# Performance work log

Hardware: AMD Instinct MI355X
Metric: run time of the kernel (lower is better)

Reference implementation:

```python
import jax, jax.numpy as jnp
import numpy as np

N = 50000      # nodes
E = 800000     # edges
F_IN = 256     # feat_dim
H = 256        # hidden dim (both layers)
L = 128        # latent dim
BN_EPS = 1e-5


def setup_inputs() -> dict:
    key = jax.random.key(0)
    ks = jax.random.split(key, 16)
    x = jax.random.normal(ks[0], (N, F_IN), dtype=jnp.float32)
    edge_index = jax.random.randint(ks[1], (2, E), 0, N, dtype=jnp.int32)
    s = 0.05
    return {
        "x": x,
        "edge_index": edge_index,
        "W0": s * jax.random.normal(ks[2], (F_IN, H), jnp.float32),
        "b0": jnp.zeros((H,), jnp.float32),
        "gamma0": jnp.ones((H,), jnp.float32),
        "beta0": jnp.zeros((H,), jnp.float32),
        "W1": s * jax.random.normal(ks[3], (H, H), jnp.float32),
        "b1": jnp.zeros((H,), jnp.float32),
        "gamma1": jnp.ones((H,), jnp.float32),
        "beta1": jnp.zeros((H,), jnp.float32),
        "W_mu": s * jax.random.normal(ks[4], (H, L), jnp.float32),
        "b_mu": jnp.zeros((L,), jnp.float32),
        "W_lv": s * jax.random.normal(ks[5], (H, L), jnp.float32),
        "b_lv": jnp.zeros((L,), jnp.float32),
    }


def _gcn_conv(h, src, dst, coef, W, b):
    # h' = W h, then symmetric-normalized scatter-add aggregation (PyG GCNConv)
    h = h @ W                                   # [N, H]
    msg = h[src] * coef                         # gather + scale, [E+N, H]
    out = jax.ops.segment_sum(msg, dst, num_segments=N)
    return out + b


def _bn(h, gamma, beta):
    # BatchNorm1d over node dimension (training-mode batch statistics)
    m = h.mean(axis=0)
    v = h.var(axis=0)
    return (h - m) * jax.lax.rsqrt(v + BN_EPS) * gamma + beta


def reference(x, edge_index, W0, b0, gamma0, beta0, W1, b1, gamma1, beta1,
              W_mu, b_mu, W_lv, b_lv):
    loops = jnp.arange(N, dtype=edge_index.dtype)
    src = jnp.concatenate([edge_index[0], loops])   # with self-loops
    dst = jnp.concatenate([edge_index[1], loops])
    deg = jax.ops.segment_sum(jnp.ones((E + N,), x.dtype), dst, num_segments=N)
    dinv = jnp.where(deg > 0, jax.lax.rsqrt(jnp.maximum(deg, 1.0)), 0.0)
    coef = (dinv[src] * dinv[dst])[:, None]          # [E+N, 1]

    h = jax.nn.relu(_bn(_gcn_conv(x, src, dst, coef, W0, b0), gamma0, beta0))
    h = jax.nn.relu(_bn(_gcn_conv(h, src, dst, coef, W1, b1), gamma1, beta1))
    # dropout is identity at inference
    mu = h @ W_mu + b_mu
    logvar = h @ W_lv + b_lv
    return mu, logvar
```

## Files before the change

### kernel.cpp

```cpp
#include <hip/hip_runtime.h>
#include <hip/hip_bf16.h>

#define NN 50000
#define NP 50001
#define NE 800000
#define FD 256
#define LD 128
#define BN_EPS 1e-5f
#define NEPAD (NE + 7 * NN + 16)

typedef __bf16 bf16_t;
typedef bf16_t bf16x8 __attribute__((ext_vector_type(8)));
typedef float f32x4 __attribute__((ext_vector_type(4)));
typedef float f32x2 __attribute__((ext_vector_type(2)));
typedef int i32x2 __attribute__((ext_vector_type(2)));
typedef int i32x4 __attribute__((ext_vector_type(4)));
typedef unsigned int u32x4 __attribute__((ext_vector_type(4)));
typedef unsigned short u16x8 __attribute__((ext_vector_type(8)));


__global__ __launch_bounds__(256) void k_count(const int* __restrict__ dst,
                                               int* __restrict__ cnt) {
  int i = blockIdx.x * blockDim.x + threadIdx.x;
  if (i < NE) atomicAdd(&cnt[dst[i]], 1);
}

__global__ __launch_bounds__(256) void k_scanA(const int* __restrict__ cnt,
                                               int* __restrict__ row_ptr,
                                               int* __restrict__ partials) {
  __shared__ int ws[4];
  int b = blockIdx.x, t = threadIdx.x;
  int base = b * 1024 + t * 4;
  int vals[4];
#pragma unroll
  for (int j = 0; j < 4; ++j)
    vals[j] = (base + j < NN) ? ((cnt[base + j] + 7) & ~7) : 0;
  int tsum = vals[0] + vals[1] + vals[2] + vals[3];
  int lane = t & 63, wid = t >> 6;
  int x = tsum;
#pragma unroll
  for (int off = 1; off < 64; off <<= 1) {
    int y = __shfl_up(x, off, 64);
    if (lane >= off) x += y;
  }
  if (lane == 63) ws[wid] = x;
  __syncthreads();
  int woff = 0;
  for (int w = 0; w < wid; ++w) woff += ws[w];
  int run = woff + x - tsum;
#pragma unroll
  for (int j = 0; j < 4; ++j) {
    if (base + j < NN) row_ptr[base + j] = run;
    run += vals[j];
  }
  if (t == 255) partials[b] = woff + x;
}

__global__ void k_scanB(int* __restrict__ partials, int* __restrict__ row_ptr,
                        int nblk) {
  int lane = threadIdx.x;
  int v = (lane < nblk) ? partials[lane] : 0;
  int x = v;
#pragma unroll
  for (int off = 1; off < 64; off <<= 1) {
    int y = __shfl_up(x, off, 64);
    if (lane >= off) x += y;
  }
  if (lane < nblk) partials[lane] = x - v;
  if (lane == nblk - 1) row_ptr[NN] = x;
}

__global__ __launch_bounds__(256) void k_scanC(int* __restrict__ row_ptr,
                                               const int* __restrict__ partials,
                                               const int* __restrict__ cnt,
                                               float* __restrict__ dinv,
                                               unsigned short* __restrict__ col,
                                               int* __restrict__ hist) {
  __shared__ int lh[64];
  int b = blockIdx.x, t = threadIdx.x;
  if (t < 64) lh[t] = 0;
  __syncthreads();
  int off = partials[b];
  int base = b * 1024 + t * 4;
#pragma unroll
  for (int j = 0; j < 4; ++j)
    if (base + j < NN) {
      int deg = cnt[base + j];
      int rp = row_ptr[base + j] + off;
      row_ptr[base + j] = rp;
      dinv[base + j] = rsqrtf(1.0f + (float)deg);
      int pd = (deg + 7) & ~7;
      for (int p = deg; p < pd; ++p) col[rp + p] = (unsigned short)NN;
      int it = pd >> 3;
      if (it > 63) it = 63;
      atomicAdd(&lh[it], 1);
    }
  __syncthreads();
  if (t < 64 && lh[t]) atomicAdd(&hist[t], lh[t]);
}

__global__ __launch_bounds__(256) void k_fill(const int* __restrict__ src,
                                              const int* __restrict__ dst,
                                              const int* __restrict__ row_ptr,
                                              int* __restrict__ cursor,
                                              unsigned short* __restrict__ col) {
  int i = blockIdx.x * blockDim.x + threadIdx.x;
  if (i < NE) {
    int d = dst[i];
    int p = atomicAdd(&cursor[d], 1);
    col[row_ptr[d] + p] = (unsigned short)src[i];
  }
}

__global__ __launch_bounds__(256) void k_order(
    const int* __restrict__ cnt, const int* __restrict__ row_ptr,
    const float* __restrict__ dinv, const int* __restrict__ hist,
    int* __restrict__ rank, int* __restrict__ order, i32x2* __restrict__ desc,
    float* __restrict__ dinvp) {
  __shared__ int lcnt[64];
  __shared__ int gbase[64];
  __shared__ int sc[64];
  int t = threadIdx.x;
  if (t < 64) {
    lcnt[t] = 0;
    int v = hist[t];
    int x = v;
#pragma unroll
    for (int off = 1; off < 64; off <<= 1) {
      int y = __shfl_up(x, off, 64);
      if (t >= off) x += y;
    }
    sc[t] = x - v;
  }
  __syncthreads();
  int i = blockIdx.x * 256 + t;
  int it = 0, rloc = 0, pd = 0;
  bool valid = (i < NN);
  if (valid) {
    pd = (cnt[i] + 7) & ~7;
    it = pd >> 3;
    if (it > 63) it = 63;
    rloc = atomicAdd(&lcnt[it], 1);
  }
  __syncthreads();
  if (t < 64 && lcnt[t]) gbase[t] = sc[t] + atomicAdd(&rank[t], lcnt[t]);
  __syncthreads();
  if (valid) {
    int p = gbase[it] + rloc;
    order[p] = i;
    int rp = row_ptr[i];
    desc[p] = (i32x2){rp, rp + pd};
    dinvp[p] = dinv[i];
  }
}

__global__ __launch_bounds__(256) void k_convw(
    const float* __restrict__ W0, const float* __restrict__ W1,
    const float* __restrict__ Wmu, const float* __restrict__ bmu,
    const float* __restrict__ Wlv, const float* __restrict__ blv,
    bf16_t* __restrict__ W0s, bf16_t* __restrict__ W1s,
    bf16_t* __restrict__ Whs, float* __restrict__ biash,
    bf16_t* __restrict__ g16, bf16_t* __restrict__ agg16) {
  int k = blockIdx.x, n = threadIdx.x;
  int chunk = (n >> 4) * 8 + (k >> 5);
  int slot = ((k >> 3) & 3) * 16 + (n & 15);
  int idx = chunk * 512 + slot * 8 + (k & 7);
  W0s[idx] = (bf16_t)W0[k * 256 + n];
  W1s[idx] = (bf16_t)W1[k * 256 + n];
  float wh = (n < 128) ? Wmu[k * 128 + n] : Wlv[k * 128 + (n - 128)];
  Whs[idx] = (bf16_t)wh;
  if (k == 0) biash[n] = (n < 128) ? bmu[n] : blv[n - 128];
  if (k == 1) {
    int ss = n >> 6, j = n & 63;
    g16[((size_t)ss * NP + NN) * 64 + j] = (bf16_t)0.f;
    agg16[((size_t)ss * NP + NN) * 64 + j] = (bf16_t)0.f;
  }
}

__global__ __launch_bounds__(256) void k_mgemm(
    const void* __restrict__ Ap, int a_f32, const bf16_t* __restrict__ Wswz,
    bf16_t* __restrict__ Cb, float* __restrict__ Cf, int M,
    const float* __restrict__ stats, const float* __restrict__ gamma,
    const float* __restrict__ beta, const float* __restrict__ row_scale,
    const float* __restrict__ col_bias, int split) {
  __shared__ float bnsc_l[256], bnsh_l[256];
  const int tid = threadIdx.x;
  const int half = blockIdx.y;
  if (stats) {
    float mean = stats[tid] * (1.0f / NN);
    float var = stats[256 + tid] * (1.0f / NN) - mean * mean;
    float rs = rsqrtf(var + BN_EPS);
    float sc = gamma[tid] * rs;
    bnsc_l[tid] = sc;
    bnsh_l[tid] = beta[tid] - mean * sc;
    __syncthreads();
  }

  const int wave = tid >> 6, lane = tid & 63;
  const int m = lane & 15, q = lane >> 4;
  const int row0 = blockIdx.x * 64 + wave * 16;
  const int rg = row0 + m;
  const int rc = rg < M ? rg : M - 1;

  bf16x8 af[8];
  if (a_f32) {
    const float* p = (const float*)Ap + (size_t)rc * 256 + q * 8;
    float4 f0[8], f1[8];
#pragma unroll
    for (int kb = 0; kb < 8; ++kb) {
      f0[kb] = *(const float4*)(p + kb * 32);
      f1[kb] = *(const float4*)(p + kb * 32 + 4);
    }
#pragma unroll
    for (int kb = 0; kb < 8; ++kb) {
      bf16x8 fr;
      fr[0] = (bf16_t)f0[kb].x; fr[1] = (bf16_t)f0[kb].y;
      fr[2] = (bf16_t)f0[kb].z; fr[3] = (bf16_t)f0[kb].w;
      fr[4] = (bf16_t)f1[kb].x; fr[5] = (bf16_t)f1[kb].y;
      fr[6] = (bf16_t)f1[kb].z; fr[7] = (bf16_t)f1[kb].w;
      af[kb] = fr;
    }
  } else {
    const bf16_t* pA = (const bf16_t*)Ap;
    bf16x8 raw[8];
#pragma unroll
    for (int kb = 0; kb < 8; ++kb)
      raw[kb] = *(const bf16x8*)&pA[((size_t)(kb >> 1) * NP + rc) * 64 +
                                    (kb & 1) * 32 + q * 8];
#pragma unroll
    for (int kb = 0; kb < 8; ++kb) {
      float s[8], h[8];
      if (stats) {
        float4 s0 = *(const float4*)&bnsc_l[kb * 32 + q * 8];
        float4 s1 = *(const float4*)&bnsc_l[kb * 32 + q * 8 + 4];
        float4 h0 = *(const float4*)&bnsh_l[kb * 32 + q * 8];
        float4 h1 = *(const float4*)&bnsh_l[kb * 32 + q * 8 + 4];
        s[0] = s0.x; s[1] = s0.y; s[2] = s0.z; s[3] = s0.w;
        s[4] = s1.x; s[5] = s1.y; s[6] = s1.z; s[7] = s1.w;
        h[0] = h0.x; h[1] = h0.y; h[2] = h0.z; h[3] = h0.w;
        h[4] = h1.x; h[5] = h1.y; h[6] = h1.z; h[7] = h1.w;
      }
      bf16x8 r = raw[kb];
      bf16x8 fr;
#pragma unroll
      for (int j = 0; j < 8; ++j) {
        float v = (float)r[j];
        if (stats) v = fmaxf(fmaf(v, s[j], h[j]), 0.f);
        fr[j] = (bf16_t)v;
      }
      af[kb] = fr;
    }
  }

  const bf16_t* Wb = Wswz + (size_t)half * 64 * 512 + lane * 8;
  f32x4 acc[8] = {};
#pragma unroll
  for (int nt = 0; nt < 8; ++nt) {
#pragma unroll
    for (int kb = 0; kb < 8; ++kb) {
      bf16x8 b = *(const bf16x8*)&Wb[(nt * 8 + kb) * 512];
      acc[nt] =
          __builtin_amdgcn_mfma_f32_16x16x32_bf16(af[kb], b, acc[nt], 0, 0, 0);
    }
  }

#pragma unroll
  for (int r = 0; r < 4; ++r) {
    int row = row0 + q * 4 + r;
    if (row >= M) continue;
    float rs = row_scale ? row_scale[row] : 1.0f;
#pragma unroll
    for (int nt = 0; nt < 8; ++nt) {
      int col = half * 128 + nt * 16 + m;
      float v = acc[nt][r] * rs;
      if (col_bias) v += col_bias[col];
      if (Cb) {
        Cb[((size_t)(col >> 6) * NP + row) * 64 + (col & 63)] = (bf16_t)v;
      } else if (!split) {
        Cf[(size_t)row * 256 + col] = v;
      } else {
        if (col < 128)
          Cf[(size_t)row * 128 + col] = v;
        else
          Cf[(size_t)(M + row) * 128 + (col - 128)] = v;
      }
    }
  }
}

#define ACCUM8(A, d)                                             \
  A[0] += (f32x2){__uint_as_float(d[0] << 16),                   \
                  __uint_as_float(d[0] & 0xffff0000u)};          \
  A[1] += (f32x2){__uint_as_float(d[1] << 16),                   \
                  __uint_as_float(d[1] & 0xffff0000u)};          \
  A[2] += (f32x2){__uint_as_float(d[2] << 16),                   \
                  __uint_as_float(d[2] & 0xffff0000u)};          \
  A[3] += (f32x2){__uint_as_float(d[3] << 16),                   \
                  __uint_as_float(d[3] & 0xffff0000u)};

__global__ __launch_bounds__(256) void k_spmm(
    const bf16_t* __restrict__ g, const int* __restrict__ order,
    const i32x2* __restrict__ desc, const unsigned short* __restrict__ col,
    const float* __restrict__ dinvp, bf16_t* __restrict__ out,
    float* __restrict__ stats) {
  __shared__ float sbuf[32][64];
  const int s = blockIdx.x & 3;
  const int grp = blockIdx.x >> 2;
  const int team = threadIdx.x >> 3, tl = threadIdx.x & 7;
  const int slotA = grp * 64 + team * 2;
  const u32x4* gu = (const u32x4*)(g + (size_t)s * NP * 64);
  float s1[8] = {}, s2[8] = {};
  if (slotA < NN) {
    f32x2 accA[4] = {}, accB[4] = {};
    i32x2 o2 = *(const i32x2*)&order[slotA];
    i32x4 d4 = *(const i32x4*)&desc[slotA];
    f32x2 dv2 = *(const f32x2*)&dinvp[slotA];
    int dstA = o2[0], dstB = o2[1];
    int bA = d4[0], eA = d4[1], bB = d4[2], eB = d4[3];
    {
      u32x4 dA = gu[(size_t)dstA * 8 + tl];
      u32x4 dB = gu[(size_t)dstB * 8 + tl];
      ACCUM8(accA, dA)
      ACCUM8(accB, dB)
    }
    u16x8 cA = {}, cB = {};
    if (bA < eA) cA = __builtin_nontemporal_load((const u16x8*)&col[bA]);
    if (bB < eB) cB = __builtin_nontemporal_load((const u16x8*)&col[bB]);
    while (bA < eA && bB < eB) {
      u32x4 wa0 = gu[(size_t)cA[0] * 8 + tl];
      u32x4 wa1 = gu[(size_t)cA[1] * 8 + tl];
      u32x4 wa2 = gu[(size_t)cA[2] * 8 + tl];
      u32x4 wa3 = gu[(size_t)cA[3] * 8 + tl];
      u32x4 wa4 = gu[(size_t)cA[4] * 8 + tl];
      u32x4 wa5 = gu[(size_t)cA[5] * 8 + tl];
      u32x4 wa6 = gu[(size_t)cA[6] * 8 + tl];
      u32x4 wa7 = gu[(size_t)cA[7] * 8 + tl];
      u32x4 wb0 = gu[(size_t)cB[0] * 8 + tl];
      u32x4 wb1 = gu[(size_t)cB[1] * 8 + tl];
      u32x4 wb2 = gu[(size_t)cB[2] * 8 + tl];
      u32x4 wb3 = gu[(size_t)cB[3] * 8 + tl];
      u32x4 wb4 = gu[(size_t)cB[4] * 8 + tl];
      u32x4 wb5 = gu[(size_t)cB[5] * 8 + tl];
      u32x4 wb6 = gu[(size_t)cB[6] * 8 + tl];
      u32x4 wb7 = gu[(size_t)cB[7] * 8 + tl];
      int bnA = bA + 8, bnB = bB + 8;
      u16x8 cnA = {}, cnB = {};
      if (bnA < eA) cnA = __builtin_nontemporal_load((const u16x8*)&col[bnA]);
      if (bnB < eB) cnB = __builtin_nontemporal_load((const u16x8*)&col[bnB]);
      ACCUM8(accA, wa0) ACCUM8(accA, wa1) ACCUM8(accA, wa2) ACCUM8(accA, wa3)
      ACCUM8(accA, wa4) ACCUM8(accA, wa5) ACCUM8(accA, wa6) ACCUM8(accA, wa7)
      ACCUM8(accB, wb0) ACCUM8(accB, wb1) ACCUM8(accB, wb2) ACCUM8(accB, wb3)
      ACCUM8(accB, wb4) ACCUM8(accB, wb5) ACCUM8(accB, wb6) ACCUM8(accB, wb7)
      cA = cnA;
      cB = cnB;
      bA = bnA;
      bB = bnB;
    }
    while (bA < eA) {
      u32x4 w0 = gu[(size_t)cA[0] * 8 + tl];
      u32x4 w1 = gu[(size_t)cA[1] * 8 + tl];
      u32x4 w2 = gu[(size_t)cA[2] * 8 + tl];
      u32x4 w3 = gu[(size_t)cA[3] * 8 + tl];
      u32x4 w4 = gu[(size_t)cA[4] * 8 + tl];
      u32x4 w5 = gu[(size_t)cA[5] * 8 + tl];
      u32x4 w6 = gu[(size_t)cA[6] * 8 + tl];
      u32x4 w7 = gu[(size_t)cA[7] * 8 + tl];
      int bn = bA + 8;
      u16x8 cn = {};
      if (bn < eA) cn = __builtin_nontemporal_load((const u16x8*)&col[bn]);
      ACCUM8(accA, w0) ACCUM8(accA, w1) ACCUM8(accA, w2) ACCUM8(accA, w3)
      ACCUM8(accA, w4) ACCUM8(accA, w5) ACCUM8(accA, w6) ACCUM8(accA, w7)
      cA = cn;
      bA = bn;
    }
    while (bB < eB) {
      u32x4 w0 = gu[(size_t)cB[0] * 8 + tl];
      u32x4 w1 = gu[(size_t)cB[1] * 8 + tl];
      u32x4 w2 = gu[(size_t)cB[2] * 8 + tl];
      u32x4 w3 = gu[(size_t)cB[3] * 8 + tl];
      u32x4 w4 = gu[(size_t)cB[4] * 8 + tl];
      u32x4 w5 = gu[(size_t)cB[5] * 8 + tl];
      u32x4 w6 = gu[(size_t)cB[6] * 8 + tl];
      u32x4 w7 = gu[(size_t)cB[7] * 8 + tl];
      int bn = bB + 8;
      u16x8 cn = {};
      if (bn < eB) cn = __builtin_nontemporal_load((const u16x8*)&col[bn]);
      ACCUM8(accB, w0) ACCUM8(accB, w1) ACCUM8(accB, w2) ACCUM8(accB, w3)
      ACCUM8(accB, w4) ACCUM8(accB, w5) ACCUM8(accB, w6) ACCUM8(accB, w7)
      cB = cn;
      bB = bn;
    }
    float dvA = dv2[0], dvB = dv2[1];
    bf16x8 ovA, ovB;
#pragma unroll
    for (int j = 0; j < 8; ++j) {
      ovA[j] = (bf16_t)(accA[j >> 1][j & 1] * dvA);
      ovB[j] = (bf16_t)(accB[j >> 1][j & 1] * dvB);
    }
    __builtin_nontemporal_store(
        ovA, (bf16x8*)&out[((size_t)s * NP + dstA) * 64 + (size_t)tl * 8]);
    __builtin_nontemporal_store(
        ovB, (bf16x8*)&out[((size_t)s * NP + dstB) * 64 + (size_t)tl * 8]);
#pragma unroll
    for (int j = 0; j < 8; ++j) {
      float va = (float)ovA[j], vb = (float)ovB[j];
      s1[j] += va + vb;
      s2[j] = fmaf(va, va, s2[j]);
      s2[j] = fmaf(vb, vb, s2[j]);
    }
  }
#pragma unroll
  for (int j = 0; j < 8; ++j) sbuf[team][tl * 8 + j] = s1[j];
  __syncthreads();
  if (threadIdx.x < 64) {
    float tot = 0.f;
#pragma unroll
    for (int w = 0; w < 32; ++w) tot += sbuf[w][threadIdx.x];
    atomicAdd(&stats[s * 64 + threadIdx.x], tot);
  }
  __syncthreads();
#pragma unroll
  for (int j = 0; j < 8; ++j) sbuf[team][tl * 8 + j] = s2[j];
  __syncthreads();
  if (threadIdx.x < 64) {
    float tot = 0.f;
#pragma unroll
    for (int w = 0; w < 32; ++w) tot += sbuf[w][threadIdx.x];
    atomicAdd(&stats[256 + s * 64 + threadIdx.x], tot);
  }
}

extern "C" void kernel_launch(void* const* d_in, const int* in_sizes, int n_in,
                              void* d_out, int out_size, void* d_ws, size_t ws_size,
                              hipStream_t stream) {
  const float* x = (const float*)d_in[0];
  const int* ei = (const int*)d_in[1];
  const int* esrc = ei;
  const int* edst = ei + NE;
  const float* W0 = (const float*)d_in[2];
  const float* gamma0 = (const float*)d_in[4];
  const float* beta0 = (const float*)d_in[5];
  const float* W1 = (const float*)d_in[6];
  const float* gamma1 = (const float*)d_in[8];
  const float* beta1 = (const float*)d_in[9];
  const float* W_mu = (const float*)d_in[10];
  const float* b_mu = (const float*)d_in[11];
  const float* W_lv = (const float*)d_in[12];
  const float* b_lv = (const float*)d_in[13];
  float* out = (float*)d_out;

  bf16_t* g16 = (bf16_t*)d_ws;
  bf16_t* agg16 = g16 + (size_t)4 * NP * 64;
  int* cnt = (int*)(agg16 + (size_t)4 * NP * 64);
  int* cursor = cnt + NN;
  float* statsAll = (float*)(cursor + NN);
  int* hist = (int*)(statsAll + 1024);
  int* rank = hist + 64;
  float* dinv = (float*)(rank + 64);
  float* biash = dinv + NN;
  bf16_t* W0s = (bf16_t*)(biash + 256);
  bf16_t* W1s = W0s + 256 * 256;
  bf16_t* Whs = W1s + 256 * 256;
  int* row_ptr = (int*)(Whs + 256 * 256);
  int* order = row_ptr + NN + 4;
  float* dinvp = (float*)(order + NN);
  i32x2* desc = (i32x2*)(dinvp + NN);
  unsigned short* col = (unsigned short*)(desc + NN);
  int* partials = (int*)(col + NEPAD);

  const int SCAN_BLKS = (NN + 1023) / 1024;

  hipMemsetAsync(cnt, 0, (2 * NN + 1024 + 128) * sizeof(int), stream);
  k_count<<<(NE + 255) / 256, 256, 0, stream>>>(edst, cnt);
  k_scanA<<<SCAN_BLKS, 256, 0, stream>>>(cnt, row_ptr, partials);
  k_scanB<<<1, 64, 0, stream>>>(partials, row_ptr, SCAN_BLKS);
  k_scanC<<<SCAN_BLKS, 256, 0, stream>>>(row_ptr, partials, cnt, dinv, col,
                                         hist);
  k_fill<<<(NE + 255) / 256, 256, 0, stream>>>(esrc, edst, row_ptr, cursor, col);
  k_order<<<(NN + 255) / 256, 256, 0, stream>>>(cnt, row_ptr, dinv, hist, rank,
                                                order, desc, dinvp);
  k_convw<<<256, 256, 0, stream>>>(W0, W1, W_mu, b_mu, W_lv, b_lv, W0s, W1s,
                                   Whs, biash, g16, agg16);

  dim3 gg((NN + 63) / 64, 2);
  const int SPMM_BLKS = 4 * ((NN + 63) / 64);

  k_mgemm<<<gg, 256, 0, stream>>>(x, 1, W0s, g16, nullptr, NN, nullptr, nullptr,
                                  nullptr, dinv, nullptr, 0);
  k_spmm<<<SPMM_BLKS, 256, 0, stream>>>(g16, order, desc, col, dinvp, agg16,
                                        statsAll);

  k_mgemm<<<gg, 256, 0, stream>>>(agg16, 0, W1s, g16, nullptr, NN, statsAll,
                                  gamma0, beta0, dinv, nullptr, 0);
  k_spmm<<<SPMM_BLKS, 256, 0, stream>>>(g16, order, desc, col, dinvp, agg16,
                                        statsAll + 512);

  k_mgemm<<<gg, 256, 0, stream>>>(agg16, 0, Whs, nullptr, out, NN,
                                  statsAll + 512, gamma1, beta1, nullptr, biash,
                                  1);
}
```

Measured before the change: 402.3 us.

## Fuse CSR build preprocessing kernels into one cooperative grid-synced kernel

```diff
diff --git a/kernel.cpp b/kernel.cpp
--- a/kernel.cpp
+++ b/kernel.cpp
@@ -1,5 +1,8 @@
 #include <hip/hip_runtime.h>
 #include <hip/hip_bf16.h>
+#include <hip/hip_cooperative_groups.h>
+
+namespace cg = cooperative_groups;
 
 #define NN 50000
 #define NP 50001
@@ -18,162 +21,149 @@
 typedef unsigned int u32x4 __attribute__((ext_vector_type(4)));
 typedef unsigned short u16x8 __attribute__((ext_vector_type(8)));
 
-
-__global__ __launch_bounds__(256) void k_count(const int* __restrict__ dst,
-                                               int* __restrict__ cnt) {
-  int i = blockIdx.x * blockDim.x + threadIdx.x;
-  if (i < NE) atomicAdd(&cnt[dst[i]], 1);
-}
-
-__global__ __launch_bounds__(256) void k_scanA(const int* __restrict__ cnt,
-                                               int* __restrict__ row_ptr,
-                                               int* __restrict__ partials) {
-  __shared__ int ws[4];
-  int b = blockIdx.x, t = threadIdx.x;
-  int base = b * 1024 + t * 4;
-  int vals[4];
-#pragma unroll
-  for (int j = 0; j < 4; ++j)
-    vals[j] = (base + j < NN) ? ((cnt[base + j] + 7) & ~7) : 0;
-  int tsum = vals[0] + vals[1] + vals[2] + vals[3];
-  int lane = t & 63, wid = t >> 6;
-  int x = tsum;
-#pragma unroll
-  for (int off = 1; off < 64; off <<= 1) {
-    int y = __shfl_up(x, off, 64);
-    if (lane >= off) x += y;
-  }
-  if (lane == 63) ws[wid] = x;
+__global__ __launch_bounds__(256) void k_build(
+    const int* __restrict__ src, const int* __restrict__ dst,
+    int* __restrict__ cnt, int* __restrict__ cursor, int* __restrict__ row_ptr,
+    int* __restrict__ partials, float* __restrict__ dinv,
+    unsigned short* __restrict__ col, int* __restrict__ hist,
+    int* __restrict__ rank, int* __restrict__ order, i32x2* __restrict__ desc,
+    float* __restrict__ dinvp, const float* __restrict__ W0,
+    const float* __restrict__ W1, const float* __restrict__ Wmu,
+    const float* __restrict__ bmu, const float* __restrict__ Wlv,
+    const float* __restrict__ blv, bf16_t* __restrict__ W0s,
+    bf16_t* __restrict__ W1s, bf16_t* __restrict__ Whs,
+    float* __restrict__ biash, bf16_t* __restrict__ g16,
+    bf16_t* __restrict__ agg16) {
+  cg::grid_group grid = cg::this_grid();
+  __shared__ int s0[64], s1[64], s2[64];
+  const int t = threadIdx.x, b = blockIdx.x;
+  const int gtid = b * 256 + t;
+  const int GT = 256 * 256;
+
+  for (int i = gtid; i < 2 * NN + 1152; i += GT) cnt[i] = 0;
+  {
+    int k = b, n = t;
+    int chunk = (n >> 4) * 8 + (k >> 5);
+    int slot = ((k >> 3) & 3) * 16 + (n & 15);
+    int idx = chunk * 512 + slot * 8 + (k & 7);
+    W0s[idx] = (bf16_t)W0[k * 256 + n];
+    W1s[idx] = (bf16_t)W1[k * 256 + n];
+    float wh = (n < 128) ? Wmu[k * 128 + n] : Wlv[k * 128 + (n - 128)];
+    Whs[idx] = (bf16_t)wh;
+    if (k == 0) biash[n] = (n < 128) ? bmu[n] : blv[n - 128];
+    if (k == 1) {
+      int ss = n >> 6, j = n & 63;
+      g16[((size_t)ss * NP + NN) * 64 + j] = (bf16_t)0.f;
+      agg16[((size_t)ss * NP + NN) * 64 + j] = (bf16_t)0.f;
+    }
+  }
+  grid.sync();
+
+  for (int i = gtid; i < NE; i += GT) atomicAdd(&cnt[dst[i]], 1);
+  grid.sync();
+
+  if (b < 49) {
+    int base = b * 1024 + t * 4;
+    int vals[4];
+#pragma unroll
+    for (int j = 0; j < 4; ++j)
+      vals[j] = (base + j < NN) ? ((cnt[base + j] + 7) & ~7) : 0;
+    int tsum = vals[0] + vals[1] + vals[2] + vals[3];
+    int lane = t & 63, wid = t >> 6;
+    int x = tsum;
+#pragma unroll
+    for (int off = 1; off < 64; off <<= 1) {
+      int y = __shfl_up(x, off, 64);
+      if (lane >= off) x += y;
+    }
+    if (lane == 63) s0[wid] = x;
+    __syncthreads();
+    int woff = 0;
+    for (int w = 0; w < wid; ++w) woff += s0[w];
+    int run = woff + x - tsum;
+#pragma unroll
+    for (int j = 0; j < 4; ++j) {
+      if (base + j < NN) row_ptr[base + j] = run;
+      run += vals[j];
+    }
+    if (t == 255) partials[b] = woff + x;
+  }
+  grid.sync();
+
+  if (b == 0 && t < 64) {
+    int v = (t < 49) ? partials[t] : 0;
+    int x = v;
+#pragma unroll
+    for (int off = 1; off < 64; off <<= 1) {
+      int y = __shfl_up(x, off, 64);
+      if (t >= off) x += y;
+    }
+    if (t < 49) partials[t] = x - v;
+    if (t == 48) row_ptr[NN] = x;
+  }
+  grid.sync();
+
+  if (t < 64) s0[t] = 0;
   __syncthreads();
-  int woff = 0;
-  for (int w = 0; w < wid; ++w) woff += ws[w];
-  int run = woff + x - tsum;
-#pragma unroll
-  for (int j = 0; j < 4; ++j) {
-    if (base + j < NN) row_ptr[base + j] = run;
-    run += vals[j];
-  }
-  if (t == 255) partials[b] = woff + x;
-}
-
-__global__ void k_scanB(int* __restrict__ partials, int* __restrict__ row_ptr,
-                        int nblk) {
-  int lane = threadIdx.x;
-  int v = (lane < nblk) ? partials[lane] : 0;
-  int x = v;
-#pragma unroll
-  for (int off = 1; off < 64; off <<= 1) {
-    int y = __shfl_up(x, off, 64);
-    if (lane >= off) x += y;
-  }
-  if (lane < nblk) partials[lane] = x - v;
-  if (lane == nblk - 1) row_ptr[NN] = x;
-}
-
-__global__ __launch_bounds__(256) void k_scanC(int* __restrict__ row_ptr,
-                                               const int* __restrict__ partials,
-                                               const int* __restrict__ cnt,
-                                               float* __restrict__ dinv,
-                                               unsigned short* __restrict__ col,
-                                               int* __restrict__ hist) {
-  __shared__ int lh[64];
-  int b = blockIdx.x, t = threadIdx.x;
-  if (t < 64) lh[t] = 0;
-  __syncthreads();
-  int off = partials[b];
-  int base = b * 1024 + t * 4;
-#pragma unroll
-  for (int j = 0; j < 4; ++j)
-    if (base + j < NN) {
-      int deg = cnt[base + j];
-      int rp = row_ptr[base + j] + off;
-      row_ptr[base + j] = rp;
-      dinv[base + j] = rsqrtf(1.0f + (float)deg);
-      int pd = (deg + 7) & ~7;
-      for (int p = deg; p < pd; ++p) col[rp + p] = (unsigned short)NN;
+  if (b < 49) {
+    int off = partials[b];
+    int base = b * 1024 + t * 4;
+#pragma unroll
+    for (int j = 0; j < 4; ++j)
+      if (base + j < NN) {
+        int deg = cnt[base + j];
+        int rp = row_ptr[base + j] + off;
+        row_ptr[base + j] = rp;
+        dinv[base + j] = rsqrtf(1.0f + (float)deg);
+        int pd = (deg + 7) & ~7;
+        for (int p = deg; p < pd; ++p) col[rp + p] = (unsigned short)NN;
+        int it = pd >> 3;
+        if (it > 63) it = 63;
+        atomicAdd(&s0[63 - it], 1);
+      }
+    __syncthreads();
+    if (t < 64 && s0[t]) atomicAdd(&hist[t], s0[t]);
+  }
+  grid.sync();
+
+  {
+    if (t < 64) {
+      s0[t] = 0;
+      int v = hist[t];
+      int x = v;
+#pragma unroll
+      for (int off = 1; off < 64; off <<= 1) {
+        int y = __shfl_up(x, off, 64);
+        if (t >= off) x += y;
+      }
+      s2[t] = x - v;
+    }
+    __syncthreads();
+    int i = gtid;
+    int bin = 0, rloc = 0, pd = 0;
+    bool valid = (i < NN);
+    if (valid) {
+      pd = (cnt[i] + 7) & ~7;
       int it = pd >> 3;
       if (it > 63) it = 63;
-      atomicAdd(&lh[it], 1);
-    }
-  __syncthreads();
-  if (t < 64 && lh[t]) atomicAdd(&hist[t], lh[t]);
-}
-
-__global__ __launch_bounds__(256) void k_fill(const int* __restrict__ src,
-                                              const int* __restrict__ dst,
-                                              const int* __restrict__ row_ptr,
-                                              int* __restrict__ cursor,
-                                              unsigned short* __restrict__ col) {
-  int i = blockIdx.x * blockDim.x + threadIdx.x;
-  if (i < NE) {
+      bin = 63 - it;
+      rloc = atomicAdd(&s0[bin], 1);
+    }
+    __syncthreads();
+    if (t < 64 && s0[t]) s1[t] = s2[t] + atomicAdd(&rank[t], s0[t]);
+    __syncthreads();
+    if (valid) {
+      int p = s1[bin] + rloc;
+      order[p] = i;
+      int rp = row_ptr[i];
+      desc[p] = (i32x2){rp, rp + pd};
+      dinvp[p] = dinv[i];
+    }
+  }
+  for (int i = gtid; i < NE; i += GT) {
     int d = dst[i];
     int p = atomicAdd(&cursor[d], 1);
     col[row_ptr[d] + p] = (unsigned short)src[i];
-  }
-}
-
-__global__ __launch_bounds__(256) void k_order(
-    const int* __restrict__ cnt, const int* __restrict__ row_ptr,
-    const float* __restrict__ dinv, const int* __restrict__ hist,
-    int* __restrict__ rank, int* __restrict__ order, i32x2* __restrict__ desc,
-    float* __restrict__ dinvp) {
-  __shared__ int lcnt[64];
-  __shared__ int gbase[64];
-  __shared__ int sc[64];
-  int t = threadIdx.x;
-  if (t < 64) {
-    lcnt[t] = 0;
-    int v = hist[t];
-    int x = v;
-#pragma unroll
-    for (int off = 1; off < 64; off <<= 1) {
-      int y = __shfl_up(x, off, 64);
-      if (t >= off) x += y;
-    }
-    sc[t] = x - v;
-  }
-  __syncthreads();
-  int i = blockIdx.x * 256 + t;
-  int it = 0, rloc = 0, pd = 0;
-  bool valid = (i < NN);
-  if (valid) {
-    pd = (cnt[i] + 7) & ~7;
-    it = pd >> 3;
-    if (it > 63) it = 63;
-    rloc = atomicAdd(&lcnt[it], 1);
-  }
-  __syncthreads();
-  if (t < 64 && lcnt[t]) gbase[t] = sc[t] + atomicAdd(&rank[t], lcnt[t]);
-  __syncthreads();
-  if (valid) {
-    int p = gbase[it] + rloc;
-    order[p] = i;
-    int rp = row_ptr[i];
-    desc[p] = (i32x2){rp, rp + pd};
-    dinvp[p] = dinv[i];
-  }
-}
-
-__global__ __launch_bounds__(256) void k_convw(
-    const float* __restrict__ W0, const float* __restrict__ W1,
-    const float* __restrict__ Wmu, const float* __restrict__ bmu,
-    const float* __restrict__ Wlv, const float* __restrict__ blv,
-    bf16_t* __restrict__ W0s, bf16_t* __restrict__ W1s,
-    bf16_t* __restrict__ Whs, float* __restrict__ biash,
-    bf16_t* __restrict__ g16, bf16_t* __restrict__ agg16) {
-  int k = blockIdx.x, n = threadIdx.x;
-  int chunk = (n >> 4) * 8 + (k >> 5);
-  int slot = ((k >> 3) & 3) * 16 + (n & 15);
-  int idx = chunk * 512 + slot * 8 + (k & 7);
-  W0s[idx] = (bf16_t)W0[k * 256 + n];
-  W1s[idx] = (bf16_t)W1[k * 256 + n];
-  float wh = (n < 128) ? Wmu[k * 128 + n] : Wlv[k * 128 + (n - 128)];
-  Whs[idx] = (bf16_t)wh;
-  if (k == 0) biash[n] = (n < 128) ? bmu[n] : blv[n - 128];
-  if (k == 1) {
-    int ss = n >> 6, j = n & 63;
-    g16[((size_t)ss * NP + NN) * 64 + j] = (bf16_t)0.f;
-    agg16[((size_t)ss * NP + NN) * 64 + j] = (bf16_t)0.f;
   }
 }
 
@@ -468,19 +458,14 @@
   unsigned short* col = (unsigned short*)(desc + NN);
   int* partials = (int*)(col + NEPAD);
 
-  const int SCAN_BLKS = (NN + 1023) / 1024;
-
-  hipMemsetAsync(cnt, 0, (2 * NN + 1024 + 128) * sizeof(int), stream);
-  k_count<<<(NE + 255) / 256, 256, 0, stream>>>(edst, cnt);
-  k_scanA<<<SCAN_BLKS, 256, 0, stream>>>(cnt, row_ptr, partials);
-  k_scanB<<<1, 64, 0, stream>>>(partials, row_ptr, SCAN_BLKS);
-  k_scanC<<<SCAN_BLKS, 256, 0, stream>>>(row_ptr, partials, cnt, dinv, col,
-                                         hist);
-  k_fill<<<(NE + 255) / 256, 256, 0, stream>>>(esrc, edst, row_ptr, cursor, col);
-  k_order<<<(NN + 255) / 256, 256, 0, stream>>>(cnt, row_ptr, dinv, hist, rank,
-                                                order, desc, dinvp);
-  k_convw<<<256, 256, 0, stream>>>(W0, W1, W_mu, b_mu, W_lv, b_lv, W0s, W1s,
-                                   Whs, biash, g16, agg16);
+  {
+    void* args[] = {&esrc, &edst, &cnt,   &cursor, &row_ptr, &partials, &dinv,
+                    &col,  &hist, &rank,  &order,  &desc,    &dinvp,    &W0,
+                    &W1,   &W_mu, &b_mu,  &W_lv,   &b_lv,    &W0s,      &W1s,
+                    &Whs,  &biash, &g16,  &agg16};
+    hipLaunchCooperativeKernel((void*)k_build, dim3(256), dim3(256), args, 0,
+                               stream);
+  }
 
   dim3 gg((NN + 63) / 64, 2);
   const int SPMM_BLKS = 4 * ((NN + 63) / 64);
```

New measurement: 553.6 us. 37.6% more time.

## Fuse CSR build kernels, single-block scan, stage GEMM weights in LDS

Applied to the files above, without the earlier changes.

```diff
diff --git a/kernel.cpp b/kernel.cpp
--- a/kernel.cpp
+++ b/kernel.cpp
@@ -8,6 +8,8 @@
 #define LD 128
 #define BN_EPS 1e-5f
 #define NEPAD (NE + 7 * NN + 16)
+#define CNT_BLKS 3125
+#define ORD_BLKS 196
 
 typedef __bf16 bf16_t;
 typedef bf16_t bf16x8 __attribute__((ext_vector_type(8)));
@@ -18,187 +20,178 @@
 typedef unsigned int u32x4 __attribute__((ext_vector_type(4)));
 typedef unsigned short u16x8 __attribute__((ext_vector_type(8)));
 
-
-__global__ __launch_bounds__(256) void k_count(const int* __restrict__ dst,
-                                               int* __restrict__ cnt) {
-  int i = blockIdx.x * blockDim.x + threadIdx.x;
-  if (i < NE) atomicAdd(&cnt[dst[i]], 1);
-}
-
-__global__ __launch_bounds__(256) void k_scanA(const int* __restrict__ cnt,
-                                               int* __restrict__ row_ptr,
-                                               int* __restrict__ partials) {
-  __shared__ int ws[4];
-  int b = blockIdx.x, t = threadIdx.x;
-  int base = b * 1024 + t * 4;
-  int vals[4];
-#pragma unroll
-  for (int j = 0; j < 4; ++j)
-    vals[j] = (base + j < NN) ? ((cnt[base + j] + 7) & ~7) : 0;
-  int tsum = vals[0] + vals[1] + vals[2] + vals[3];
-  int lane = t & 63, wid = t >> 6;
-  int x = tsum;
-#pragma unroll
-  for (int off = 1; off < 64; off <<= 1) {
-    int y = __shfl_up(x, off, 64);
-    if (lane >= off) x += y;
-  }
-  if (lane == 63) ws[wid] = x;
-  __syncthreads();
-  int woff = 0;
-  for (int w = 0; w < wid; ++w) woff += ws[w];
-  int run = woff + x - tsum;
-#pragma unroll
-  for (int j = 0; j < 4; ++j) {
-    if (base + j < NN) row_ptr[base + j] = run;
-    run += vals[j];
-  }
-  if (t == 255) partials[b] = woff + x;
-}
-
-__global__ void k_scanB(int* __restrict__ partials, int* __restrict__ row_ptr,
-                        int nblk) {
-  int lane = threadIdx.x;
-  int v = (lane < nblk) ? partials[lane] : 0;
-  int x = v;
-#pragma unroll
-  for (int off = 1; off < 64; off <<= 1) {
-    int y = __shfl_up(x, off, 64);
-    if (lane >= off) x += y;
-  }
-  if (lane < nblk) partials[lane] = x - v;
-  if (lane == nblk - 1) row_ptr[NN] = x;
-}
-
-__global__ __launch_bounds__(256) void k_scanC(int* __restrict__ row_ptr,
-                                               const int* __restrict__ partials,
-                                               const int* __restrict__ cnt,
-                                               float* __restrict__ dinv,
-                                               unsigned short* __restrict__ col,
-                                               int* __restrict__ hist) {
-  __shared__ int lh[64];
-  int b = blockIdx.x, t = threadIdx.x;
-  if (t < 64) lh[t] = 0;
-  __syncthreads();
-  int off = partials[b];
-  int base = b * 1024 + t * 4;
-#pragma unroll
-  for (int j = 0; j < 4; ++j)
-    if (base + j < NN) {
-      int deg = cnt[base + j];
-      int rp = row_ptr[base + j] + off;
-      row_ptr[base + j] = rp;
-      dinv[base + j] = rsqrtf(1.0f + (float)deg);
-      int pd = (deg + 7) & ~7;
-      for (int p = deg; p < pd; ++p) col[rp + p] = (unsigned short)NN;
-      int it = pd >> 3;
-      if (it > 63) it = 63;
-      atomicAdd(&lh[it], 1);
-    }
-  __syncthreads();
-  if (t < 64 && lh[t]) atomicAdd(&hist[t], lh[t]);
-}
-
-__global__ __launch_bounds__(256) void k_fill(const int* __restrict__ src,
-                                              const int* __restrict__ dst,
-                                              const int* __restrict__ row_ptr,
-                                              int* __restrict__ cursor,
-                                              unsigned short* __restrict__ col) {
-  int i = blockIdx.x * blockDim.x + threadIdx.x;
-  if (i < NE) {
-    int d = dst[i];
-    int p = atomicAdd(&cursor[d], 1);
-    col[row_ptr[d] + p] = (unsigned short)src[i];
-  }
-}
-
-__global__ __launch_bounds__(256) void k_order(
-    const int* __restrict__ cnt, const int* __restrict__ row_ptr,
-    const float* __restrict__ dinv, const int* __restrict__ hist,
-    int* __restrict__ rank, int* __restrict__ order, i32x2* __restrict__ desc,
-    float* __restrict__ dinvp) {
-  __shared__ int lcnt[64];
-  __shared__ int gbase[64];
-  __shared__ int sc[64];
-  int t = threadIdx.x;
-  if (t < 64) {
-    lcnt[t] = 0;
-    int v = hist[t];
-    int x = v;
-#pragma unroll
-    for (int off = 1; off < 64; off <<= 1) {
-      int y = __shfl_up(x, off, 64);
-      if (t >= off) x += y;
-    }
-    sc[t] = x - v;
-  }
-  __syncthreads();
-  int i = blockIdx.x * 256 + t;
-  int it = 0, rloc = 0, pd = 0;
-  bool valid = (i < NN);
-  if (valid) {
-    pd = (cnt[i] + 7) & ~7;
-    it = pd >> 3;
-    if (it > 63) it = 63;
-    rloc = atomicAdd(&lcnt[it], 1);
-  }
-  __syncthreads();
-  if (t < 64 && lcnt[t]) gbase[t] = sc[t] + atomicAdd(&rank[t], lcnt[t]);
-  __syncthreads();
-  if (valid) {
-    int p = gbase[it] + rloc;
-    order[p] = i;
-    int rp = row_ptr[i];
-    desc[p] = (i32x2){rp, rp + pd};
-    dinvp[p] = dinv[i];
-  }
-}
-
-__global__ __launch_bounds__(256) void k_convw(
+__global__ __launch_bounds__(256) void k_countw(
+    const int* __restrict__ dst, int* __restrict__ cnt,
     const float* __restrict__ W0, const float* __restrict__ W1,
     const float* __restrict__ Wmu, const float* __restrict__ bmu,
     const float* __restrict__ Wlv, const float* __restrict__ blv,
     bf16_t* __restrict__ W0s, bf16_t* __restrict__ W1s,
     bf16_t* __restrict__ Whs, float* __restrict__ biash,
     bf16_t* __restrict__ g16, bf16_t* __restrict__ agg16) {
-  int k = blockIdx.x, n = threadIdx.x;
-  int chunk = (n >> 4) * 8 + (k >> 5);
-  int slot = ((k >> 3) & 3) * 16 + (n & 15);
-  int idx = chunk * 512 + slot * 8 + (k & 7);
-  W0s[idx] = (bf16_t)W0[k * 256 + n];
-  W1s[idx] = (bf16_t)W1[k * 256 + n];
-  float wh = (n < 128) ? Wmu[k * 128 + n] : Wlv[k * 128 + (n - 128)];
-  Whs[idx] = (bf16_t)wh;
-  if (k == 0) biash[n] = (n < 128) ? bmu[n] : blv[n - 128];
-  if (k == 1) {
-    int ss = n >> 6, j = n & 63;
-    g16[((size_t)ss * NP + NN) * 64 + j] = (bf16_t)0.f;
-    agg16[((size_t)ss * NP + NN) * 64 + j] = (bf16_t)0.f;
-  }
-}
-
-__global__ __launch_bounds__(256) void k_mgemm(
+  int b = blockIdx.x, t = threadIdx.x;
+  if (b < CNT_BLKS) {
+    int i = b * 256 + t;
+    if (i < NE) atomicAdd(&cnt[dst[i]], 1);
+  } else {
+    int k = b - CNT_BLKS, n = t;
+    int chunk = (n >> 4) * 8 + (k >> 5);
+    int slot = ((k >> 3) & 3) * 16 + (n & 15);
+    int idx = chunk * 512 + slot * 8 + (k & 7);
+    W0s[idx] = (bf16_t)W0[k * 256 + n];
+    W1s[idx] = (bf16_t)W1[k * 256 + n];
+    float wh = (n < 128) ? Wmu[k * 128 + n] : Wlv[k * 128 + (n - 128)];
+    Whs[idx] = (bf16_t)wh;
+    if (k == 0) biash[n] = (n < 128) ? bmu[n] : blv[n - 128];
+    if (k == 1) {
+      int ss = n >> 6, j = n & 63;
+      g16[((size_t)ss * NP + NN) * 64 + j] = (bf16_t)0.f;
+      agg16[((size_t)ss * NP + NN) * 64 + j] = (bf16_t)0.f;
+    }
+  }
+}
+
+__global__ __launch_bounds__(1024) void k_scan(const int* __restrict__ cnt,
+                                               int* __restrict__ row_ptr,
+                                               float* __restrict__ dinv,
+                                               unsigned short* __restrict__ col,
+                                               int* __restrict__ binoff) {
+  __shared__ int ws[16];
+  __shared__ int hist_l[64];
+  int t = threadIdx.x;
+  if (t < 64) hist_l[t] = 0;
+  __syncthreads();
+  int carry = 0;
+  for (int c = 0; c < 13; ++c) {
+    int base = c * 4096 + t * 4;
+    int degs[4], vals[4];
+#pragma unroll
+    for (int j = 0; j < 4; ++j) {
+      degs[j] = (base + j < NN) ? cnt[base + j] : 0;
+      vals[j] = (degs[j] + 7) & ~7;
+      if (base + j >= NN) vals[j] = 0;
+    }
+    int tsum = vals[0] + vals[1] + vals[2] + vals[3];
+    int lane = t & 63, wid = t >> 6;
+    int x = tsum;
+#pragma unroll
+    for (int off = 1; off < 64; off <<= 1) {
+      int y = __shfl_up(x, off, 64);
+      if (lane >= off) x += y;
+    }
+    if (lane == 63) ws[wid] = x;
+    __syncthreads();
+    int woff = 0, total = 0;
+#pragma unroll
+    for (int w = 0; w < 16; ++w) {
+      int v = ws[w];
+      if (w < wid) woff += v;
+      total += v;
+    }
+    int run = carry + woff + x - tsum;
+#pragma unroll
+    for (int j = 0; j < 4; ++j) {
+      if (base + j < NN) {
+        int deg = degs[j];
+        row_ptr[base + j] = run;
+        dinv[base + j] = rsqrtf(1.0f + (float)deg);
+        int pd = vals[j];
+        for (int p = deg; p < pd; ++p) col[run + p] = (unsigned short)NN;
+        int it = pd >> 3;
+        if (it > 63) it = 63;
+        atomicAdd(&hist_l[63 - it], 1);
+        run += pd;
+      }
+    }
+    carry += total;
+    __syncthreads();
+  }
+  if (t < 64) {
+    int v = hist_l[t];
+    int x = v;
+#pragma unroll
+    for (int off = 1; off < 64; off <<= 1) {
+      int y = __shfl_up(x, off, 64);
+      if (t >= off) x += y;
+    }
+    binoff[t] = x - v;
+  }
+}
+
+__global__ __launch_bounds__(256) void k_fillorder(
+    const int* __restrict__ src, const int* __restrict__ dst,
+    const int* __restrict__ row_ptr, int* __restrict__ cursor,
+    unsigned short* __restrict__ col, const int* __restrict__ cnt,
+    const float* __restrict__ dinv, const int* __restrict__ binoff,
+    int* __restrict__ rank, int* __restrict__ order, i32x2* __restrict__ desc,
+    float* __restrict__ dinvp) {
+  int b = blockIdx.x, t = threadIdx.x;
+  if (b < CNT_BLKS) {
+    int i = b * 256 + t;
+    if (i < NE) {
+      int d = dst[i];
+      int p = atomicAdd(&cursor[d], 1);
+      col[row_ptr[d] + p] = (unsigned short)src[i];
+    }
+  } else {
+    __shared__ int lcnt[64];
+    __shared__ int gbase[64];
+    if (t < 64) lcnt[t] = 0;
+    __syncthreads();
+    int i = (b - CNT_BLKS) * 256 + t;
+    int bin = 0, rloc = 0, pd = 0;
+    bool valid = (i < NN);
+    if (valid) {
+      pd = (cnt[i] + 7) & ~7;
+      int it = pd >> 3;
+      if (it > 63) it = 63;
+      bin = 63 - it;
+      rloc = atomicAdd(&lcnt[bin], 1);
+    }
+    __syncthreads();
+    if (t < 64 && lcnt[t]) gbase[t] = binoff[t] + atomicAdd(&rank[t], lcnt[t]);
+    __syncthreads();
+    if (valid) {
+      int p = gbase[bin] + rloc;
+      order[p] = i;
+      int rp = row_ptr[i];
+      desc[p] = (i32x2){rp, rp + pd};
+      dinvp[p] = dinv[i];
+    }
+  }
+}
+
+__global__ __launch_bounds__(512) void k_mgemm(
     const void* __restrict__ Ap, int a_f32, const bf16_t* __restrict__ Wswz,
     bf16_t* __restrict__ Cb, float* __restrict__ Cf, int M,
     const float* __restrict__ stats, const float* __restrict__ gamma,
     const float* __restrict__ beta, const float* __restrict__ row_scale,
     const float* __restrict__ col_bias, int split) {
+  __shared__ bf16_t Ws[64 * 512];
   __shared__ float bnsc_l[256], bnsh_l[256];
   const int tid = threadIdx.x;
   const int half = blockIdx.y;
-  if (stats) {
+  {
+    const bf16_t* srcW = Wswz + (size_t)half * 64 * 512;
+    bf16x8 wraw[8];
+#pragma unroll
+    for (int i = 0; i < 8; ++i)
+      wraw[i] = *(const bf16x8*)&srcW[(i * 512 + tid) * 8];
+#pragma unroll
+    for (int i = 0; i < 8; ++i) *(bf16x8*)&Ws[(i * 512 + tid) * 8] = wraw[i];
+  }
+  if (stats && tid < 256) {
     float mean = stats[tid] * (1.0f / NN);
     float var = stats[256 + tid] * (1.0f / NN) - mean * mean;
     float rs = rsqrtf(var + BN_EPS);
     float sc = gamma[tid] * rs;
     bnsc_l[tid] = sc;
     bnsh_l[tid] = beta[tid] - mean * sc;
-    __syncthreads();
-  }
+  }
+  __syncthreads();
 
   const int wave = tid >> 6, lane = tid & 63;
   const int m = lane & 15, q = lane >> 4;
-  const int row0 = blockIdx.x * 64 + wave * 16;
+  const int row0 = blockIdx.x * 128 + wave * 16;
   const int rg = row0 + m;
   const int rc = rg < M ? rg : M - 1;
 
@@ -252,13 +245,12 @@
     }
   }
 
-  const bf16_t* Wb = Wswz + (size_t)half * 64 * 512 + lane * 8;
   f32x4 acc[8] = {};
 #pragma unroll
   for (int nt = 0; nt < 8; ++nt) {
 #pragma unroll
     for (int kb = 0; kb < 8; ++kb) {
-      bf16x8 b = *(const bf16x8*)&Wb[(nt * 8 + kb) * 512];
+      bf16x8 b = *(const bf16x8*)&Ws[(nt * 8 + kb) * 512 + lane * 8];
       acc[nt] =
           __builtin_amdgcn_mfma_f32_16x16x32_bf16(af[kb], b, acc[nt], 0, 0, 0);
     }
@@ -466,36 +458,31 @@
   float* dinvp = (float*)(order + NN);
   i32x2* desc = (i32x2*)(dinvp + NN);
   unsigned short* col = (unsigned short*)(desc + NN);
-  int* partials = (int*)(col + NEPAD);
-
-  const int SCAN_BLKS = (NN + 1023) / 1024;
+  int* binoff = (int*)(col + NEPAD);
 
   hipMemsetAsync(cnt, 0, (2 * NN + 1024 + 128) * sizeof(int), stream);
-  k_count<<<(NE + 255) / 256, 256, 0, stream>>>(edst, cnt);
-  k_scanA<<<SCAN_BLKS, 256, 0, stream>>>(cnt, row_ptr, partials);
-  k_scanB<<<1, 64, 0, stream>>>(partials, row_ptr, SCAN_BLKS);
-  k_scanC<<<SCAN_BLKS, 256, 0, stream>>>(row_ptr, partials, cnt, dinv, col,
-                                         hist);
-  k_fill<<<(NE + 255) / 256, 256, 0, stream>>>(esrc, edst, row_ptr, cursor, col);
-  k_order<<<(NN + 255) / 256, 256, 0, stream>>>(cnt, row_ptr, dinv, hist, rank,
-                                                order, desc, dinvp);
-  k_convw<<<256, 256, 0, stream>>>(W0, W1, W_mu, b_mu, W_lv, b_lv, W0s, W1s,
-                                   Whs, biash, g16, agg16);
-
-  dim3 gg((NN + 63) / 64, 2);
+  k_countw<<<CNT_BLKS + 256, 256, 0, stream>>>(edst, cnt, W0, W1, W_mu, b_mu,
+                                               W_lv, b_lv, W0s, W1s, Whs,
+                                               biash, g16, agg16);
+  k_scan<<<1, 1024, 0, stream>>>(cnt, row_ptr, dinv, col, binoff);
+  k_fillorder<<<CNT_BLKS + ORD_BLKS, 256, 0, stream>>>(
+      esrc, edst, row_ptr, cursor, col, cnt, dinv, binoff, rank, order, desc,
+      dinvp);
+
+  dim3 gg((NN + 127) / 128, 2);
   const int SPMM_BLKS = 4 * ((NN + 63) / 64);
 
-  k_mgemm<<<gg, 256, 0, stream>>>(x, 1, W0s, g16, nullptr, NN, nullptr, nullptr,
+  k_mgemm<<<gg, 512, 0, stream>>>(x, 1, W0s, g16, nullptr, NN, nullptr, nullptr,
                                   nullptr, dinv, nullptr, 0);
   k_spmm<<<SPMM_BLKS, 256, 0, stream>>>(g16, order, desc, col, dinvp, agg16,
                                         statsAll);
 
-  k_mgemm<<<gg, 256, 0, stream>>>(agg16, 0, W1s, g16, nullptr, NN, statsAll,
+  k_mgemm<<<gg, 512, 0, stream>>>(agg16, 0, W1s, g16, nullptr, NN, statsAll,
                                   gamma0, beta0, dinv, nullptr, 0);
   k_spmm<<<SPMM_BLKS, 256, 0, stream>>>(g16, order, desc, col, dinvp, agg16,
                                         statsAll + 512);
 
-  k_mgemm<<<gg, 256, 0, stream>>>(agg16, 0, Whs, nullptr, out, NN,
+  k_mgemm<<<gg, 512, 0, stream>>>(agg16, 0, Whs, nullptr, out, NN,
                                   statsAll + 512, gamma1, beta1, nullptr, biash,
                                   1);
 }
```

After: 458.7 us. 1.14x slower.
